# Optimization experiments

Measured on AMD Instinct MI355X. Metric: run time of the kernel, lower is better.

Reference implementation:

```python
import jax, jax.numpy as jnp
import numpy as np

S, P, T, E, H = 32, 48, 8, 64, 64      # scenes, peds/scene, obs_len, embedding_dim, h_dim
D1, D2 = 512, 1024                      # mlp_pre_pool hidden / bottleneck dims
B = S * P
TOTAL_LEN = 20                          # obs_len + pred_len (8 + 12)


def setup_inputs() -> dict:
    key = jax.random.key(0)
    ks = jax.random.split(key, 10)
    h_states = jax.random.normal(ks[0], (1, B, H), jnp.float32)
    end_pos = jax.random.normal(ks[1], (B, 2), jnp.float32)
    traj = jax.random.normal(ks[2], (TOTAL_LEN, B, 2), jnp.float32)
    traj_weight = jax.random.uniform(ks[3], (S, P * P, 2, T), jnp.float32)
    starts = jnp.arange(S, dtype=jnp.int32) * P
    seq_start_end = jnp.stack([starts, starts + P], axis=1)  # uniform scenes of P peds
    # learned params
    W_se = jax.random.normal(ks[4], (T * E, 2 * T), jnp.float32) * 0.05  # spatial_embedding
    b_se = jnp.zeros((T * E,), jnp.float32)
    W1 = jax.random.normal(ks[5], (D1, T * E + H), jnp.float32) * 0.05   # 576 -> 512
    b1 = jnp.zeros((D1,), jnp.float32)
    W2 = jax.random.normal(ks[6], (D2, D1), jnp.float32) * 0.05          # 512 -> 1024
    b2 = jnp.zeros((D2,), jnp.float32)
    return {"h_states": h_states, "seq_start_end": seq_start_end, "end_pos": end_pos,
            "traj": traj, "traj_weight": traj_weight, "mlp_pre_pool_dim_0": T * E,
            "W_se": W_se, "b_se": b_se, "W1": W1, "b1": b1, "W2": W2, "b2": b2}


def reference(h_states, seq_start_end, end_pos, traj, traj_weight, mlp_pre_pool_dim_0,
              W_se, b_se, W1, b1, W2, b2):
    # obs_traj: (obs_len, B, 2) -> (B, T, 2) -> per-scene (S, P, T, 2)
    obs = traj[:T].transpose(1, 0, 2).reshape(S, P, T, 2)
    h = h_states.reshape(S, P, H)
    # pairwise history differences: row (i, j) = obs[j] - obs[i]  (gather-diff)
    rel = obs[:, None, :, :, :] - obs[:, :, None, :, :]          # (S, i, j, T, 2)
    rel = rel.reshape(S, P, P, 2 * T)                            # flatten (T,2) -> 2T
    emb = rel @ W_se.T + b_se                                    # (S, P, P, T*E)
    # traj_weight[i]: (P*P, 2, T) -> permute(0,2,1) -> tile channel to E -> flatten
    w = jnp.transpose(traj_weight, (0, 1, 3, 2))                 # (S, P*P, T, 2)
    w = jnp.tile(w, (1, 1, 1, E // 2)).reshape(S, P, P, T * E)
    emb = w * emb
    # curr_hidden_1: hidden of ped j broadcast over i
    hj = jnp.broadcast_to(h[:, None, :, :], (S, P, P, H))
    x = jnp.concatenate([emb, hj], axis=-1)                      # (S, P, P, 576)
    x = jax.nn.relu(x @ W1.T + b1)                               # (S, P, P, 512)
    x = jax.nn.relu(x @ W2.T + b2)                               # (S, P, P, 1024)
    pool_h = x.max(axis=2)                                       # max over j
    return pool_h.reshape(S * P, D2)
```

## Files before the change

### kernel.cpp

```cpp
#include <hip/hip_runtime.h>
#include <hip/hip_bf16.h>
#include <stdint.h>

#define S_  32
#define P_  48
#define T_  8
#define E_  64
#define H_  64
#define D1_ 512
#define D2_ 1024
#define B_  (S_*P_)
#define M_  (S_*P_*P_)
#define K1_ 576
#define KE_ 512

typedef __attribute__((ext_vector_type(8))) short  short8;
typedef __attribute__((ext_vector_type(8))) __bf16 bf16x8;
typedef __attribute__((ext_vector_type(4))) float  f32x4;
typedef __attribute__((ext_vector_type(8))) float  f32x8;

__device__ inline short f2bf(float x) {
  union { float f; unsigned u; } v; v.f = x;
  unsigned r = v.u + 0x7FFFu + ((v.u >> 16) & 1u);
  return (short)(r >> 16);
}

__device__ inline void async16(const void* g, void* l) {
  __builtin_amdgcn_global_load_lds(
      (const __attribute__((address_space(1))) void*)g,
      (__attribute__((address_space(3))) void*)l, 16, 0, 0);
}

__device__ inline f32x4 mfma16(short8 a, short8 b, f32x4 c) {
  return __builtin_amdgcn_mfma_f32_16x16x32_bf16(
      __builtin_bit_cast(bf16x8, a), __builtin_bit_cast(bf16x8, b), c, 0, 0, 0);
}

__global__ __launch_bounds__(256) void k_cvt_w(const float* __restrict__ W1,
                                               const float* __restrict__ W2,
                                               short* __restrict__ W1b,
                                               short* __restrict__ W2b) {
  int idx = blockIdx.x * 256 + threadIdx.x;
  if (idx < D1_ * K1_) W1b[idx] = f2bf(W1[idx]);
  int idx2 = idx - D1_ * K1_;
  if (idx2 >= 0 && idx2 < D2_ * D1_) W2b[idx2] = f2bf(W2[idx2]);
}

__global__ __launch_bounds__(256) void k_oW(const float* __restrict__ traj,
                                            const float* __restrict__ Wse,
                                            float* __restrict__ oW) {
  int bid = blockIdx.x;
  int p = bid >> 1;
  int n = ((bid & 1) << 8) + threadIdx.x;
  float obs[16];
#pragma unroll
  for (int t = 0; t < T_; ++t) {
    obs[2*t]   = traj[(t*B_ + p)*2 + 0];
    obs[2*t+1] = traj[(t*B_ + p)*2 + 1];
  }
  float acc = 0.f;
#pragma unroll
  for (int k = 0; k < 16; ++k) acc += obs[k] * Wse[n*16 + k];
  oW[p*KE_ + n] = acc;
}

__global__ __launch_bounds__(256) void k_build_x(const float* __restrict__ tw,
                                                 const float* __restrict__ h,
                                                 const float* __restrict__ bse,
                                                 const float* __restrict__ oW,
                                                 short* __restrict__ X) {
  int tid = threadIdx.x;
  int wid = tid >> 6, lane = tid & 63;
  int row = blockIdx.x * 4 + wid;
  int s   = row / (P_ * P_);
  int rem = row - s * (P_ * P_);
  int i   = rem / P_;
  int j   = rem - i * P_;
  int bi = s * P_ + i, bj = s * P_ + j;

  const float* twq = tw + (size_t)(s * (P_*P_) + rem) * 16;
  int t = lane >> 3;
  float w0 = twq[t];
  float w1 = twq[8 + t];

  int n0 = lane * 8;
  f32x8 vj = *(const f32x8*)&oW[(size_t)bj * KE_ + n0];
  f32x8 vi = *(const f32x8*)&oW[(size_t)bi * KE_ + n0];
  f32x8 vb = *(const f32x8*)&bse[n0];
  short8 o;
#pragma unroll
  for (int k = 0; k < 8; ++k) {
    float e = (vj[k] - vi[k] + vb[k]) * ((k & 1) ? w1 : w0);
    o[k] = f2bf(e);
  }
  *(short8*)&X[(size_t)row * K1_ + n0] = o;

  if (lane < 8) {
    f32x8 vh = *(const f32x8*)&h[(size_t)bj * H_ + lane * 8];
    short8 oh;
#pragma unroll
    for (int k = 0; k < 8; ++k) oh[k] = f2bf(vh[k]);
    *(short8*)&X[(size_t)row * K1_ + KE_ + lane * 8] = oh;
  }
}

__global__ __launch_bounds__(512, 2) void k_gemm1(const short* __restrict__ X,
                                                  const short* __restrict__ W1b,
                                                  const float* __restrict__ b1,
                                                  short* __restrict__ X1) {
  __shared__ short Abuf[2][128 * 64];
  __shared__ short Bbuf[3][256 * 64];
  int tid = threadIdx.x;
  int wid = tid >> 6, lane = tid & 63;
  int wgid = (blockIdx.x & 7) * 144 + (blockIdx.x >> 3);
  int tm = wgid >> 1, tn = wgid & 1;
  int brow = tm * 128, bcol = tn * 256;
  int wr = wid >> 2, wc = wid & 3;
  int lr = lane & 15, lhi = lane >> 4;
  int sx = lr & 7;

  f32x4 acc[4][4];
#pragma unroll
  for (int m = 0; m < 4; ++m)
#pragma unroll
    for (int n = 0; n < 4; ++n) acc[m][n] = (f32x4){0.f, 0.f, 0.f, 0.f};

  auto stageA = [&](int buf, int k0) {
#pragma unroll
    for (int it = 0; it < 2; ++it) {
      int fg = it * 512 + tid;
      int r = fg >> 3, gs = (fg & 7) ^ (r & 7);
      async16(&X[(size_t)(brow + r) * K1_ + k0 + (gs << 3)], &Abuf[buf][fg * 8]);
    }
  };
  auto stageB = [&](int buf, int k0) {
#pragma unroll
    for (int it = 0; it < 4; ++it) {
      int fg = it * 512 + tid;
      int r = fg >> 3, gs = (fg & 7) ^ (r & 7);
      async16(&W1b[(size_t)(bcol + r) * K1_ + k0 + (gs << 3)], &Bbuf[buf][fg * 8]);
    }
  };
  auto compute = [&](int bA, int bB) {
#pragma unroll
    for (int kk = 0; kk < 2; ++kk) {
      int gr = kk * 4 + lhi;
      short8 a[4], b[4];
#pragma unroll
      for (int m = 0; m < 4; ++m)
        a[m] = *(const short8*)&Abuf[bA][(wr*64 + m*16 + lr) * 64 + ((gr ^ sx) << 3)];
#pragma unroll
      for (int n = 0; n < 4; ++n)
        b[n] = *(const short8*)&Bbuf[bB][(wc*64 + n*16 + lr) * 64 + ((gr ^ sx) << 3)];
      __builtin_amdgcn_s_setprio(1);
#pragma unroll
      for (int m = 0; m < 4; ++m)
#pragma unroll
        for (int n = 0; n < 4; ++n)
          acc[m][n] = mfma16(a[m], b[n], acc[m][n]);
      __builtin_amdgcn_s_setprio(0);
    }
  };

  const int NT = 9;
  stageA(0, 0); stageB(0, 0); stageB(1, 64);
  asm volatile("s_waitcnt vmcnt(4)" ::: "memory");
  __builtin_amdgcn_s_barrier();
#pragma unroll
  for (int t = 0; t < NT; ++t) {
    if (t + 1 < NT) stageA((t + 1) & 1, (t + 1) * 64);
    if (t + 2 < NT) stageB((t + 2) % 3, (t + 2) * 64);
    compute(t & 1, t % 3);
    if (t + 2 < NT)      { asm volatile("s_waitcnt vmcnt(4)" ::: "memory"); }
    else if (t + 1 < NT) { asm volatile("s_waitcnt vmcnt(0)" ::: "memory"); }
    if (t + 1 < NT) __builtin_amdgcn_s_barrier();
  }

#pragma unroll
  for (int n = 0; n < 4; ++n) {
    int gcol = bcol + wc*64 + n*16 + lr;
    float bias = b1[gcol];
#pragma unroll
    for (int m = 0; m < 4; ++m) {
      int grow0 = brow + wr*64 + m*16 + lhi*4;
#pragma unroll
      for (int q = 0; q < 4; ++q) {
        float v = acc[m][n][q] + bias;
        v = v > 0.f ? v : 0.f;
        X1[(size_t)(grow0 + q) * D1_ + gcol] = f2bf(v);
      }
    }
  }
}

__global__ __launch_bounds__(512, 2) void k_gemm2(const short* __restrict__ X1,
                                                  const short* __restrict__ W2b,
                                                  const float* __restrict__ b2,
                                                  float* __restrict__ out) {
  __shared__ short Abuf[2][192 * 64];
  __shared__ short Bbuf[3][256 * 64];
  int tid = threadIdx.x;
  int wid = tid >> 6, lane = tid & 63;
  int wgid = (blockIdx.x & 7) * 192 + (blockIdx.x >> 3);
  int tm = wgid >> 2, tn = wgid & 3;
  int brow = tm * 192, bcol = tn * 256;
  int wr = wid >> 2, wc = wid & 3;
  int lr = lane & 15, lhi = lane >> 4;
  int sx = lr & 7;

  f32x4 acc[6][4];
#pragma unroll
  for (int m = 0; m < 6; ++m)
#pragma unroll
    for (int n = 0; n < 4; ++n) acc[m][n] = (f32x4){0.f, 0.f, 0.f, 0.f};

  auto stageA = [&](int buf, int k0) {
#pragma unroll
    for (int it = 0; it < 3; ++it) {
      int fg = it * 512 + tid;
      int r = fg >> 3, gs = (fg & 7) ^ (r & 7);
      async16(&X1[(size_t)(brow + r) * D1_ + k0 + (gs << 3)], &Abuf[buf][fg * 8]);
    }
  };
  auto stageB = [&](int buf, int k0) {
#pragma unroll
    for (int it = 0; it < 4; ++it) {
      int fg = it * 512 + tid;
      int r = fg >> 3, gs = (fg & 7) ^ (r & 7);
      async16(&W2b[(size_t)(bcol + r) * D1_ + k0 + (gs << 3)], &Bbuf[buf][fg * 8]);
    }
  };
  auto compute = [&](int bA, int bB) {
#pragma unroll
    for (int kk = 0; kk < 2; ++kk) {
      int gr = kk * 4 + lhi;
      short8 a[6], b[4];
#pragma unroll
      for (int m = 0; m < 6; ++m)
        a[m] = *(const short8*)&Abuf[bA][(wr*96 + m*16 + lr) * 64 + ((gr ^ sx) << 3)];
#pragma unroll
      for (int n = 0; n < 4; ++n)
        b[n] = *(const short8*)&Bbuf[bB][(wc*64 + n*16 + lr) * 64 + ((gr ^ sx) << 3)];
      __builtin_amdgcn_s_setprio(1);
#pragma unroll
      for (int m = 0; m < 6; ++m)
#pragma unroll
        for (int n = 0; n < 4; ++n)
          acc[m][n] = mfma16(a[m], b[n], acc[m][n]);
      __builtin_amdgcn_s_setprio(0);
    }
  };

  const int NT = 8;
  stageA(0, 0); stageB(0, 0); stageB(1, 64);
  asm volatile("s_waitcnt vmcnt(4)" ::: "memory");
  __builtin_amdgcn_s_barrier();
#pragma unroll
  for (int t = 0; t < NT; ++t) {
    if (t + 1 < NT) stageA((t + 1) & 1, (t + 1) * 64);
    if (t + 2 < NT) stageB((t + 2) % 3, (t + 2) * 64);
    compute(t & 1, t % 3);
    if (t + 2 < NT)      { asm volatile("s_waitcnt vmcnt(4)" ::: "memory"); }
    else if (t + 1 < NT) { asm volatile("s_waitcnt vmcnt(0)" ::: "memory"); }
    if (t + 1 < NT) __builtin_amdgcn_s_barrier();
  }

  int gbase = tm * 4 + wr * 2;
#pragma unroll
  for (int n = 0; n < 4; ++n) {
    int gcol = bcol + wc*64 + n*16 + lr;
    float bias = b2[gcol];
    float r0 = 0.f, r1 = 0.f;
#pragma unroll
    for (int m = 0; m < 3; ++m)
#pragma unroll
      for (int q = 0; q < 4; ++q) {
        float v0 = acc[m][n][q] + bias;
        float v1 = acc[m + 3][n][q] + bias;
        if (v0 > r0) r0 = v0;
        if (v1 > r1) r1 = v1;
      }
    r0 = fmaxf(r0, __shfl_xor(r0, 16));
    r0 = fmaxf(r0, __shfl_xor(r0, 32));
    r1 = fmaxf(r1, __shfl_xor(r1, 16));
    r1 = fmaxf(r1, __shfl_xor(r1, 32));
    if (lhi == 0) {
      out[(size_t)gbase       * D2_ + gcol] = r0;
      out[(size_t)(gbase + 1) * D2_ + gcol] = r1;
    }
  }
}

extern "C" void kernel_launch(void* const* d_in, const int* in_sizes, int n_in,
                              void* d_out, int out_size, void* d_ws, size_t ws_size,
                              hipStream_t stream) {
  const float* h_states = (const float*)d_in[0];
  const float* traj = (const float*)d_in[3];
  const float* tw   = (const float*)d_in[4];
  const float* Wse  = (const float*)d_in[6];
  const float* bse  = (const float*)d_in[7];
  const float* W1   = (const float*)d_in[8];
  const float* b1   = (const float*)d_in[9];
  const float* W2   = (const float*)d_in[10];
  const float* b2   = (const float*)d_in[11];
  float* out = (float*)d_out;

  char* ws = (char*)d_ws;
  const size_t X_BYTES   = (size_t)M_ * K1_ * 2;
  const size_t X1_BYTES  = (size_t)M_ * D1_ * 2;
  const size_t W1B_BYTES = (size_t)D1_ * K1_ * 2;
  short* X   = (short*)ws;
  short* X1  = (short*)(ws + X_BYTES);
  short* W1b = (short*)(ws + X_BYTES + X1_BYTES);
  short* W2b = (short*)(ws + X_BYTES + X1_BYTES + W1B_BYTES);
  float* oW  = (float*)(ws + X_BYTES);

  k_cvt_w  <<<(D1_*K1_ + D2_*D1_ + 255) / 256, 256, 0, stream>>>(W1, W2, W1b, W2b);
  k_oW     <<<B_ * 2, 256, 0, stream>>>(traj, Wse, oW);
  k_build_x<<<M_ / 4, 256, 0, stream>>>(tw, h_states, bse, oW, X);
  k_gemm1  <<<(M_ / 128) * (D1_ / 256), 512, 0, stream>>>(X, W1b, b1, X1);
  k_gemm2  <<<(M_ / 192) * (D2_ / 256), 512, 0, stream>>>(X1, W2b, b2, out);
}
```

Baseline: 258.4 us.

## Interleave LDS reads, global prefetch and MFMA phases with barrier-fenced scheduling in both GEMMs

GEMM1 moves from 512-thread 128x256 tiles with a triple-buffered B to 256-thread 128x128 tiles with double buffering. Its main loop is split into two half-K phases, each doing LDS reads, issuing one global prefetch, then an lgkmcnt fence and an MFMA burst. GEMM2 keeps its tiling but splits each K step into four barrier-separated phases that interleave LDS reads, half-sized B prefetches and MFMA groups. The aim is a ping-pong style schedule where memory issue overlaps matrix work across waves. The cost is many more barriers per iteration, and GEMM1 now uses smaller tiles with more blocks and a shallower prefetch depth.

```diff
diff --git a/kernel.cpp b/kernel.cpp
--- a/kernel.cpp
+++ b/kernel.cpp
@@ -35,6 +35,10 @@
   return __builtin_amdgcn_mfma_f32_16x16x32_bf16(
       __builtin_bit_cast(bf16x8, a), __builtin_bit_cast(bf16x8, b), c, 0, 0, 0);
 }
+
+#define LGKM0_FENCE() do { \
+  asm volatile("s_waitcnt lgkmcnt(0)" ::: "memory"); \
+  __builtin_amdgcn_sched_barrier(0); } while (0)
 
 __global__ __launch_bounds__(256) void k_cvt_w(const float* __restrict__ W1,
                                                const float* __restrict__ W2,
@@ -104,18 +108,18 @@
   }
 }
 
-__global__ __launch_bounds__(512, 2) void k_gemm1(const short* __restrict__ X,
+__global__ __launch_bounds__(256, 2) void k_gemm1(const short* __restrict__ X,
                                                   const short* __restrict__ W1b,
                                                   const float* __restrict__ b1,
                                                   short* __restrict__ X1) {
   __shared__ short Abuf[2][128 * 64];
-  __shared__ short Bbuf[3][256 * 64];
+  __shared__ short Bbuf[2][128 * 64];
   int tid = threadIdx.x;
   int wid = tid >> 6, lane = tid & 63;
-  int wgid = (blockIdx.x & 7) * 144 + (blockIdx.x >> 3);
-  int tm = wgid >> 1, tn = wgid & 1;
-  int brow = tm * 128, bcol = tn * 256;
-  int wr = wid >> 2, wc = wid & 3;
+  int wgid = (blockIdx.x & 7) * 288 + (blockIdx.x >> 3);
+  int tm = wgid >> 2, tn = wgid & 3;
+  int brow = tm * 128, bcol = tn * 128;
+  int wr = wid >> 1, wc = wid & 1;
   int lr = lane & 15, lhi = lane >> 4;
   int sx = lr & 7;
 
@@ -127,8 +131,8 @@
 
   auto stageA = [&](int buf, int k0) {
 #pragma unroll
-    for (int it = 0; it < 2; ++it) {
-      int fg = it * 512 + tid;
+    for (int it = 0; it < 4; ++it) {
+      int fg = it * 256 + tid;
       int r = fg >> 3, gs = (fg & 7) ^ (r & 7);
       async16(&X[(size_t)(brow + r) * K1_ + k0 + (gs << 3)], &Abuf[buf][fg * 8]);
     }
@@ -136,44 +140,57 @@
   auto stageB = [&](int buf, int k0) {
 #pragma unroll
     for (int it = 0; it < 4; ++it) {
-      int fg = it * 512 + tid;
+      int fg = it * 256 + tid;
       int r = fg >> 3, gs = (fg & 7) ^ (r & 7);
       async16(&W1b[(size_t)(bcol + r) * K1_ + k0 + (gs << 3)], &Bbuf[buf][fg * 8]);
     }
   };
-  auto compute = [&](int bA, int bB) {
-#pragma unroll
-    for (int kk = 0; kk < 2; ++kk) {
-      int gr = kk * 4 + lhi;
-      short8 a[4], b[4];
-#pragma unroll
-      for (int m = 0; m < 4; ++m)
-        a[m] = *(const short8*)&Abuf[bA][(wr*64 + m*16 + lr) * 64 + ((gr ^ sx) << 3)];
+  auto dsA = [&](int buf, int kk, short8* a) {
+    int gr = kk * 4 + lhi;
+#pragma unroll
+    for (int m = 0; m < 4; ++m)
+      a[m] = *(const short8*)&Abuf[buf][(wr*64 + m*16 + lr) * 64 + ((gr ^ sx) << 3)];
+  };
+  auto dsB = [&](int buf, int kk, short8* b) {
+    int gr = kk * 4 + lhi;
+#pragma unroll
+    for (int n = 0; n < 4; ++n)
+      b[n] = *(const short8*)&Bbuf[buf][(wc*64 + n*16 + lr) * 64 + ((gr ^ sx) << 3)];
+  };
+  auto mf16 = [&](short8* a, short8* b) {
+    __builtin_amdgcn_s_setprio(1);
+#pragma unroll
+    for (int m = 0; m < 4; ++m)
 #pragma unroll
       for (int n = 0; n < 4; ++n)
-        b[n] = *(const short8*)&Bbuf[bB][(wc*64 + n*16 + lr) * 64 + ((gr ^ sx) << 3)];
-      __builtin_amdgcn_s_setprio(1);
-#pragma unroll
-      for (int m = 0; m < 4; ++m)
-#pragma unroll
-        for (int n = 0; n < 4; ++n)
-          acc[m][n] = mfma16(a[m], b[n], acc[m][n]);
-      __builtin_amdgcn_s_setprio(0);
-    }
+        acc[m][n] = mfma16(a[m], b[n], acc[m][n]);
+    __builtin_amdgcn_s_setprio(0);
   };
 
   const int NT = 9;
-  stageA(0, 0); stageB(0, 0); stageB(1, 64);
-  asm volatile("s_waitcnt vmcnt(4)" ::: "memory");
+  stageA(0, 0); stageB(0, 0);
+  asm volatile("s_waitcnt vmcnt(0)" ::: "memory");
   __builtin_amdgcn_s_barrier();
 #pragma unroll
   for (int t = 0; t < NT; ++t) {
-    if (t + 1 < NT) stageA((t + 1) & 1, (t + 1) * 64);
-    if (t + 2 < NT) stageB((t + 2) % 3, (t + 2) * 64);
-    compute(t & 1, t % 3);
-    if (t + 2 < NT)      { asm volatile("s_waitcnt vmcnt(4)" ::: "memory"); }
-    else if (t + 1 < NT) { asm volatile("s_waitcnt vmcnt(0)" ::: "memory"); }
-    if (t + 1 < NT) __builtin_amdgcn_s_barrier();
+    int bf = t & 1;
+    short8 a0[4], b0[4];
+    dsA(bf, 0, a0); dsB(bf, 0, b0);
+    if (t + 1 < NT) stageA(bf ^ 1, (t + 1) * 64);
+    __builtin_amdgcn_s_barrier();
+    LGKM0_FENCE();
+    mf16(a0, b0);
+    __builtin_amdgcn_s_barrier();
+    short8 a1[4], b1[4];
+    dsA(bf, 1, a1); dsB(bf, 1, b1);
+    if (t + 1 < NT) stageB(bf ^ 1, (t + 1) * 64);
+    __builtin_amdgcn_s_barrier();
+    LGKM0_FENCE();
+    mf16(a1, b1);
+    if (t + 1 < NT) {
+      asm volatile("s_waitcnt vmcnt(0)" ::: "memory");
+      __builtin_amdgcn_s_barrier();
+    }
   }
 
 #pragma unroll
@@ -222,44 +239,70 @@
       async16(&X1[(size_t)(brow + r) * D1_ + k0 + (gs << 3)], &Abuf[buf][fg * 8]);
     }
   };
-  auto stageB = [&](int buf, int k0) {
-#pragma unroll
-    for (int it = 0; it < 4; ++it) {
-      int fg = it * 512 + tid;
+  auto stageBh = [&](int buf, int k0, int half) {
+#pragma unroll
+    for (int it = 0; it < 2; ++it) {
+      int fg = (half * 2 + it) * 512 + tid;
       int r = fg >> 3, gs = (fg & 7) ^ (r & 7);
       async16(&W2b[(size_t)(bcol + r) * D1_ + k0 + (gs << 3)], &Bbuf[buf][fg * 8]);
     }
   };
-  auto compute = [&](int bA, int bB) {
-#pragma unroll
-    for (int kk = 0; kk < 2; ++kk) {
-      int gr = kk * 4 + lhi;
-      short8 a[6], b[4];
-#pragma unroll
-      for (int m = 0; m < 6; ++m)
-        a[m] = *(const short8*)&Abuf[bA][(wr*96 + m*16 + lr) * 64 + ((gr ^ sx) << 3)];
+  auto dsA3 = [&](int buf, int kk, int mb, short8* a) {
+    int gr = kk * 4 + lhi;
+#pragma unroll
+    for (int m = 0; m < 3; ++m)
+      a[m] = *(const short8*)&Abuf[buf][(wr*96 + (mb + m)*16 + lr) * 64 + ((gr ^ sx) << 3)];
+  };
+  auto dsB4 = [&](int buf, int kk, short8* b) {
+    int gr = kk * 4 + lhi;
+#pragma unroll
+    for (int n = 0; n < 4; ++n)
+      b[n] = *(const short8*)&Bbuf[buf][(wc*64 + n*16 + lr) * 64 + ((gr ^ sx) << 3)];
+  };
+  auto mf12 = [&](short8* a, short8* b, int mb) {
+    __builtin_amdgcn_s_setprio(1);
+#pragma unroll
+    for (int m = 0; m < 3; ++m)
 #pragma unroll
       for (int n = 0; n < 4; ++n)
-        b[n] = *(const short8*)&Bbuf[bB][(wc*64 + n*16 + lr) * 64 + ((gr ^ sx) << 3)];
-      __builtin_amdgcn_s_setprio(1);
-#pragma unroll
-      for (int m = 0; m < 6; ++m)
-#pragma unroll
-        for (int n = 0; n < 4; ++n)
-          acc[m][n] = mfma16(a[m], b[n], acc[m][n]);
-      __builtin_amdgcn_s_setprio(0);
-    }
+        acc[mb + m][n] = mfma16(a[m], b[n], acc[mb + m][n]);
+    __builtin_amdgcn_s_setprio(0);
   };
 
   const int NT = 8;
-  stageA(0, 0); stageB(0, 0); stageB(1, 64);
+  stageA(0, 0); stageBh(0, 0, 0); stageBh(0, 0, 1);
+  stageBh(1, 64, 0); stageBh(1, 64, 1);
   asm volatile("s_waitcnt vmcnt(4)" ::: "memory");
   __builtin_amdgcn_s_barrier();
 #pragma unroll
   for (int t = 0; t < NT; ++t) {
-    if (t + 1 < NT) stageA((t + 1) & 1, (t + 1) * 64);
-    if (t + 2 < NT) stageB((t + 2) % 3, (t + 2) * 64);
-    compute(t & 1, t % 3);
+    int bA = t & 1, bB = t % 3;
+    short8 a0[3], b0[4];
+    dsA3(bA, 0, 0, a0); dsB4(bB, 0, b0);
+    if (t + 1 < NT) stageA(bA ^ 1, (t + 1) * 64);
+    __builtin_amdgcn_s_barrier();
+    LGKM0_FENCE();
+    mf12(a0, b0, 0);
+    __builtin_amdgcn_s_barrier();
+    short8 a1[3];
+    dsA3(bA, 0, 3, a1);
+    if (t + 2 < NT) stageBh((t + 2) % 3, (t + 2) * 64, 0);
+    __builtin_amdgcn_s_barrier();
+    LGKM0_FENCE();
+    mf12(a1, b0, 3);
+    __builtin_amdgcn_s_barrier();
+    short8 a2[3], b1[4];
+    dsA3(bA, 1, 0, a2); dsB4(bB, 1, b1);
+    if (t + 2 < NT) stageBh((t + 2) % 3, (t + 2) * 64, 1);
+    __builtin_amdgcn_s_barrier();
+    LGKM0_FENCE();
+    mf12(a2, b1, 0);
+    __builtin_amdgcn_s_barrier();
+    short8 a3[3];
+    dsA3(bA, 1, 3, a3);
+    __builtin_amdgcn_s_barrier();
+    LGKM0_FENCE();
+    mf12(a3, b1, 3);
     if (t + 2 < NT)      { asm volatile("s_waitcnt vmcnt(4)" ::: "memory"); }
     else if (t + 1 < NT) { asm volatile("s_waitcnt vmcnt(0)" ::: "memory"); }
     if (t + 1 < NT) __builtin_amdgcn_s_barrier();
@@ -318,6 +361,6 @@
   k_cvt_w  <<<(D1_*K1_ + D2_*D1_ + 255) / 256, 256, 0, stream>>>(W1, W2, W1b, W2b);
   k_oW     <<<B_ * 2, 256, 0, stream>>>(traj, Wse, oW);
   k_build_x<<<M_ / 4, 256, 0, stream>>>(tw, h_states, bse, oW, X);
-  k_gemm1  <<<(M_ / 128) * (D1_ / 256), 512, 0, stream>>>(X, W1b, b1, X1);
+  k_gemm1  <<<(M_ / 128) * (D1_ / 128), 256, 0, stream>>>(X, W1b, b1, X1);
   k_gemm2  <<<(M_ / 192) * (D2_ / 256), 512, 0, stream>>>(X1, W2b, b2, out);
 }
```

New measurement: 248.1 us. 4.0% less time.
